# Performance work log

Hardware: AMD Instinct MI355X
Metric: run time of the kernel (lower is better)

Reference implementation:

```python
import jax, jax.numpy as jnp
import numpy as np

BN_EPS = 1e-5


def setup_inputs() -> dict:
    key = jax.random.key(0)
    k1, k2, k3, k4 = jax.random.split(key, 4)
    N, C, T, V, K = 64, 128, 300, 25, 3
    x = jax.random.normal(k1, (N, C, T, V), dtype=jnp.float32)
    A = jax.random.uniform(k2, (K, V, V), dtype=jnp.float32)
    # 1x1 conv weight (out_channels*K, in_channels) and bias
    W = jax.random.normal(k3, (C * K, C), dtype=jnp.float32) * 0.05
    b = jax.random.normal(k4, (C * K,), dtype=jnp.float32) * 0.05
    gamma = jnp.ones((C,), dtype=jnp.float32)
    beta = jnp.zeros((C,), dtype=jnp.float32)
    return {"x": x, "A": A, "W": W, "b": b, "gamma": gamma, "beta": beta}


def reference(x, A, W, b, gamma, beta):
    N, C, T, V = x.shape
    K = A.shape[0]
    # 1x1 conv: expand channels C -> K*C
    y = jnp.einsum('nctv,oc->notv', x, W) + b[None, :, None, None]
    y = y.reshape(N, K, C, T, V)
    # graph aggregation over K adjacency matrices
    y = jnp.einsum('nkctv,kvw->nctw', y, A)
    # residual + relu
    y = jax.nn.relu(y + x)
    # BatchNorm2d (training mode): stats over (N, T, V) per channel, biased var
    mean = jnp.mean(y, axis=(0, 2, 3), keepdims=True)
    var = jnp.mean(jnp.square(y - mean), axis=(0, 2, 3), keepdims=True)
    out = gamma[None, :, None, None] * (y - mean) * jax.lax.rsqrt(var + BN_EPS) + beta[None, :, None, None]
    return out, A
```

## Files before the change

### kernel.cpp

```cpp
#include <hip/hip_runtime.h>
#include <cstdint>
#include <cstddef>

#define C_    128
#define T_    300
#define V_    25
#define TT    2
#define KA    3
#define WPAD  32
#define NPOS  64
#define KDIM  384
#define B2P   392
#define ALP   40
#define XTP   40
#define NSLOT 64
#define NTOT  64

typedef __attribute__((ext_vector_type(8))) short short8;
typedef __attribute__((ext_vector_type(4))) short short4v;
typedef __attribute__((ext_vector_type(4))) float float4v;
typedef __attribute__((ext_vector_type(2))) float float2v;

__device__ __forceinline__ short f2bf(float f) {
  union { float f; uint32_t u; } v; v.f = f;
  uint32_t r = (v.u + 0x7FFFu + ((v.u >> 16) & 1u)) >> 16;
  return (short)(uint16_t)r;
}
__device__ __forceinline__ float bf2f(short s) {
  union { uint32_t u; float f; } v; v.u = ((uint32_t)(uint16_t)s) << 16;
  return v.f;
}

__global__ __launch_bounds__(256) void k0_prep(const float* __restrict__ W,
    const float* __restrict__ A, const float* __restrict__ b,
    short* __restrict__ W2, float* __restrict__ bias2, float* __restrict__ stats)
{
  int e = blockIdx.x * 256 + threadIdx.x;
  if (e < C_*KDIM) {
    int c = e / KDIM, kd = e % KDIM;
    int k = kd >> 7, c2 = kd & 127;
    W2[e] = f2bf(W[(k*C_ + c)*C_ + c2]);
  } else if (e < C_*KDIM + C_*32) {
    int i = e - C_*KDIM;
    int c = i >> 5, w = i & 31;
    float val = 0.f;
    if (w < V_) {
      for (int k = 0; k < KA; ++k) {
        float cs = 0.f;
        for (int v = 0; v < V_; ++v) cs += A[(k*V_ + v)*V_ + w];
        val += b[k*C_ + c] * cs;
      }
    }
    bias2[i] = val;
  } else if (e < C_*KDIM + C_*32 + 2*NSLOT*C_) {
    stats[e - (C_*KDIM + C_*32)] = 0.f;
  }
}

__global__ __launch_bounds__(256) void k1_main(const float* __restrict__ x,
    const float* __restrict__ A, const short* __restrict__ W2,
    const float* __restrict__ bias2, float* __restrict__ ssum,
    float* __restrict__ ssq, float* __restrict__ out)
{
  __shared__ short Albf[KA][WPAD][ALP];
  __shared__ short xt[TT][C_][XTP];
  __shared__ short B2[NPOS][B2P];

  const int tid  = threadIdx.x;
  const int lane = tid & 63;
  const int wid  = tid >> 6;
  const int l15  = lane & 15;
  const int quad = lane >> 4;
  const int nb = blockIdx.x;
  const int n  = nb / (T_/TT);
  const int tb = nb % (T_/TT);
  const int t0 = tb * TT;

  for (int i = tid; i < KA*WPAD*ALP; i += 256) {
    int k = i / (WPAD*ALP);
    int rem = i % (WPAD*ALP);
    int w = rem / ALP;
    int v = rem % ALP;
    float a = (w < V_ && v < V_) ? A[(k*V_ + v)*V_ + w] : 0.f;
    ((short*)Albf)[i] = f2bf(a);
  }
  for (int i = tid; i < TT*C_*15; i += 256) {
    int t = i / (C_*15);
    int r = i % (C_*15);
    int c = r / 15;
    int v = V_ + (r % 15);
    xt[t][c][v] = 0;
  }
  {
    const float* xb = x + (((size_t)n*C_)*T_ + t0)*V_;
    for (int p = tid; p < 3200; p += 256) {
      int c = (p*5243) >> 17;
      int r = p - c*25;
      float2v xv = *(const float2v*)(xb + (size_t)c*(T_*V_) + 2*r);
      int j0 = 2*r;
      { int j = j0;   int t = (j >= V_); int v = j - t*V_; xt[t][c][v] = f2bf(xv[0]); }
      { int j = j0+1; int t = (j >= V_); int v = j - t*V_; xt[t][c][v] = f2bf(xv[1]); }
    }
  }
  __syncthreads();

  #pragma unroll
  for (int iu = 0; iu < 3; ++iu) {
    int u  = wid*3 + iu;
    int mh = u / 6;
    int k  = (u >> 1) % 3;
    int t  = u & 1;
    short8 bf0 = *(const short8*)&Albf[k][l15][quad*8];
    short8 bf1 = *(const short8*)&Albf[k][16 + l15][quad*8];
    #pragma unroll
    for (int mi4 = 0; mi4 < 4; ++mi4) {
      int mi = mh*4 + mi4;
      int cp = mi*16 + l15;
      short8 af = *(const short8*)&xt[t][cp][quad*8];
      int c2 = k*C_ + mi*16 + quad*4;
      #pragma unroll
      for (int ni = 0; ni < 2; ++ni) {
        float4v acc = {0.f, 0.f, 0.f, 0.f};
        acc = __builtin_amdgcn_mfma_f32_16x16x32_bf16(af, ni ? bf1 : bf0, acc, 0, 0, 0);
        short4v sv;
        sv[0] = f2bf(acc[0]); sv[1] = f2bf(acc[1]);
        sv[2] = f2bf(acc[2]); sv[3] = f2bf(acc[3]);
        int pos = t*WPAD + ni*16 + l15;
        *(short4v*)&B2[pos][c2] = sv;
      }
    }
  }
  __syncthreads();

  const int wm = wid >> 1;
  const int wn = wid & 1;
  float4v acc[4][2];
  #pragma unroll
  for (int mi = 0; mi < 4; ++mi)
    #pragma unroll
    for (int ni = 0; ni < 2; ++ni)
      acc[mi][ni] = (float4v){0.f, 0.f, 0.f, 0.f};

  #pragma unroll 4
  for (int ks = 0; ks < 12; ++ks) {
    short8 bfr0 = *(const short8*)&B2[wn*32 + l15][ks*32 + quad*8];
    short8 bfr1 = *(const short8*)&B2[wn*32 + 16 + l15][ks*32 + quad*8];
    #pragma unroll
    for (int mi = 0; mi < 4; ++mi) {
      int c = wm*64 + mi*16 + l15;
      short8 afr = *(const short8*)(W2 + (size_t)c*KDIM + ks*32 + quad*8);
      acc[mi][0] = __builtin_amdgcn_mfma_f32_16x16x32_bf16(afr, bfr0, acc[mi][0], 0, 0, 0);
      acc[mi][1] = __builtin_amdgcn_mfma_f32_16x16x32_bf16(afr, bfr1, acc[mi][1], 0, 0, 0);
    }
  }

  float lsum[4][4], lsq[4][4];
  #pragma unroll
  for (int a1 = 0; a1 < 4; ++a1)
    #pragma unroll
    for (int a2 = 0; a2 < 4; ++a2) { lsum[a1][a2] = 0.f; lsq[a1][a2] = 0.f; }

  #pragma unroll
  for (int ni = 0; ni < 2; ++ni) {
    int pos = wn*32 + ni*16 + l15;
    int t = pos >> 5;
    int w = pos & 31;
    if (w < V_) {
      #pragma unroll
      for (int mi = 0; mi < 4; ++mi) {
        int cb = wm*64 + mi*16 + quad*4;
        #pragma unroll
        for (int r = 0; r < 4; ++r) {
          int cc = cb + r;
          float z = acc[mi][ni][r] + bias2[cc*32 + w];
          z += bf2f(xt[t][cc][w]);
          z = fmaxf(z, 0.f);
          acc[mi][ni][r] = z;
          lsum[mi][r] += z;
          lsq[mi][r]  += z*z;
        }
      }
    }
  }

  __syncthreads();
  float* Zs = (float*)&B2[0][0];

  #pragma unroll
  for (int ni = 0; ni < 2; ++ni) {
    int pos = wn*32 + ni*16 + l15;
    int t = pos >> 5;
    int w = pos & 31;
    if (w < V_) {
      #pragma unroll
      for (int mi = 0; mi < 4; ++mi) {
        int cb = wm*64 + mi*16 + quad*4;
        #pragma unroll
        for (int r = 0; r < 4; ++r) {
          Zs[(cb + r)*50 + t*V_ + w] = acc[mi][ni][r];
        }
      }
    }
  }
  __syncthreads();

  {
    float* ob = out + (((size_t)n*C_)*T_ + t0)*V_;
    for (int p = tid; p < 3200; p += 256) {
      int c = (p*5243) >> 17;
      int r = p - c*25;
      float2v zz = *(const float2v*)&Zs[c*50 + 2*r];
      *(float2v*)(ob + (size_t)c*(T_*V_) + 2*r) = zz;
    }
  }

  int slot = nb & (NSLOT - 1);
  #pragma unroll
  for (int mi = 0; mi < 4; ++mi) {
    #pragma unroll
    for (int r = 0; r < 4; ++r) {
      float s = lsum[mi][r];
      float q = lsq[mi][r];
      #pragma unroll
      for (int m = 1; m <= 8; m <<= 1) {
        s += __shfl_xor(s, m, 64);
        q += __shfl_xor(q, m, 64);
      }
      if (l15 == 0) {
        int cc = wm*64 + mi*16 + quad*4 + r;
        atomicAdd(&ssum[slot*C_ + cc], s);
        atomicAdd(&ssq[slot*C_ + cc], q);
      }
    }
  }
}

__global__ __launch_bounds__(256) void k2_stats(const float* __restrict__ ssum,
    const float* __restrict__ ssq, const float* __restrict__ gamma,
    const float* __restrict__ beta, const float* __restrict__ A,
    float* __restrict__ sscale, float* __restrict__ sshift, float* __restrict__ outA)
{
  int id = blockIdx.x * 256 + threadIdx.x;
  if (id < C_) {
    float s = 0.f, q = 0.f;
    for (int sl = 0; sl < NSLOT; ++sl) { s += ssum[sl*C_ + id]; q += ssq[sl*C_ + id]; }
    const float cnt = 480000.f;
    float mean = s / cnt;
    float var  = q / cnt - mean*mean;
    float inv  = rsqrtf(var + 1e-5f);
    float sc   = gamma[id] * inv;
    sscale[id] = sc;
    sshift[id] = beta[id] - mean * sc;
  } else if (id < C_ + KA*V_*V_) {
    int i = id - C_;
    outA[i] = A[i];
  }
}

__global__ __launch_bounds__(256) void k3_bn(float* __restrict__ out,
    const float* __restrict__ sscale, const float* __restrict__ sshift)
{
  __shared__ float s_sc[C_], s_sh[C_];
  int tid = threadIdx.x;
  if (tid < C_) s_sc[tid] = sscale[tid];
  else          s_sh[tid - C_] = sshift[tid - C_];
  __syncthreads();

  int n = blockIdx.x / 19;
  int chunk = blockIdx.x % 19;
  int t0c = chunk * 16;
  int tlen = (t0c + 16 <= T_) ? 16 : (T_ - t0c);
  int vlim = tlen * V_;

  for (int f = tid; f < 12800; f += 256) {
    int c = (f*5243) >> 19;
    int r = f - c*100;
    int idx0 = 4*r;
    if (idx0 >= vlim) continue;
    size_t off4 = ((size_t)n*C_*T_*V_ + (size_t)c*T_*V_ + (size_t)t0c*V_ + idx0) >> 2;
    float4v v = ((float4v*)out)[off4];
    float sc = s_sc[c], sh = s_sh[c];
    v[0] = v[0]*sc + sh; v[1] = v[1]*sc + sh;
    v[2] = v[2]*sc + sh; v[3] = v[3]*sc + sh;
    ((float4v*)out)[off4] = v;
  }
}

extern "C" void kernel_launch(void* const* d_in, const int* in_sizes, int n_in,
                              void* d_out, int out_size, void* d_ws, size_t ws_size,
                              hipStream_t stream)
{
  const float* x     = (const float*)d_in[0];
  const float* A     = (const float*)d_in[1];
  const float* W     = (const float*)d_in[2];
  const float* b     = (const float*)d_in[3];
  const float* gamma = (const float*)d_in[4];
  const float* beta  = (const float*)d_in[5];
  float* out = (float*)d_out;

  short* W2    = (short*)d_ws;
  float* bias2 = (float*)((char*)d_ws + 98304);
  float* stats = (float*)((char*)d_ws + 114688);
  float* ssum   = stats;
  float* ssq    = stats + NSLOT*C_;
  float* sscale = stats + 2*NSLOT*C_;
  float* sshift = sscale + C_;
  float* outA = out + (size_t)NTOT*C_*T_*V_;

  k0_prep <<<272,   256, 0, stream>>>(W, A, b, W2, bias2, stats);
  k1_main <<<9600,  256, 0, stream>>>(x, A, W2, bias2, ssum, ssq, out);
  k2_stats<<<8,     256, 0, stream>>>(ssum, ssq, gamma, beta, A, sscale, sshift, outA);
  k3_bn   <<<1216,  256, 0, stream>>>(out, sscale, sshift);
}
```

Baseline: 982.9 us.

## Process graph aggregation per adjacency slice to shrink LDS and raise occupancy

The k1 kernel now builds the intermediate B2 buffer one adjacency slice k at a time, 128 channels wide instead of 384. Each slice's partial GEMM is accumulated before the buffer is reused, with W2 fragments preloaded into registers per slice. This cuts shared memory use so three blocks can fit per CU (launch bounds set to 3), at the cost of extra barriers and register pressure. The BN apply kernel is also remapped to 4800 smaller blocks with a simpler index computation.

```diff
diff --git a/kernel.cpp b/kernel.cpp
--- a/kernel.cpp
+++ b/kernel.cpp
@@ -7,14 +7,17 @@
 #define V_    25
 #define TT    2
 #define KA    3
-#define WPAD  32
-#define NPOS  64
 #define KDIM  384
-#define B2P   392
+#define B2P   136
 #define ALP   40
 #define XTP   40
 #define NSLOT 64
 #define NTOT  64
+
+#define ALBF_O 0
+#define XT_O   3840
+#define B2_O   14080
+#define SH_TOT 22784
 
 typedef __attribute__((ext_vector_type(8))) short short8;
 typedef __attribute__((ext_vector_type(4))) short short4v;
@@ -57,14 +60,15 @@
   }
 }
 
-__global__ __launch_bounds__(256) void k1_main(const float* __restrict__ x,
+__global__ __launch_bounds__(256, 3) void k1_main(const float* __restrict__ x,
     const float* __restrict__ A, const short* __restrict__ W2,
     const float* __restrict__ bias2, float* __restrict__ ssum,
     float* __restrict__ ssq, float* __restrict__ out)
 {
-  __shared__ short Albf[KA][WPAD][ALP];
-  __shared__ short xt[TT][C_][XTP];
-  __shared__ short B2[NPOS][B2P];
+  __shared__ __align__(16) short SH[SH_TOT];
+  short* Albf_ = SH + ALBF_O;
+  short* xt_   = SH + XT_O;
+  short* B2_   = SH + B2_O;
 
   const int tid  = threadIdx.x;
   const int lane = tid & 63;
@@ -76,20 +80,20 @@
   const int tb = nb % (T_/TT);
   const int t0 = tb * TT;
 
-  for (int i = tid; i < KA*WPAD*ALP; i += 256) {
-    int k = i / (WPAD*ALP);
-    int rem = i % (WPAD*ALP);
+  for (int i = tid; i < KA*32*ALP; i += 256) {
+    int k = i / (32*ALP);
+    int rem = i % (32*ALP);
     int w = rem / ALP;
     int v = rem % ALP;
     float a = (w < V_ && v < V_) ? A[(k*V_ + v)*V_ + w] : 0.f;
-    ((short*)Albf)[i] = f2bf(a);
+    Albf_[i] = f2bf(a);
   }
   for (int i = tid; i < TT*C_*15; i += 256) {
     int t = i / (C_*15);
     int r = i % (C_*15);
     int c = r / 15;
     int v = V_ + (r % 15);
-    xt[t][c][v] = 0;
+    xt_[t*5120 + c*XTP + v] = 0;
   }
   {
     const float* xb = x + (((size_t)n*C_)*T_ + t0)*V_;
@@ -98,42 +102,17 @@
       int r = p - c*25;
       float2v xv = *(const float2v*)(xb + (size_t)c*(T_*V_) + 2*r);
       int j0 = 2*r;
-      { int j = j0;   int t = (j >= V_); int v = j - t*V_; xt[t][c][v] = f2bf(xv[0]); }
-      { int j = j0+1; int t = (j >= V_); int v = j - t*V_; xt[t][c][v] = f2bf(xv[1]); }
+      { int j = j0;   int t = (j >= V_); int v = j - t*V_; xt_[t*5120 + c*XTP + v] = f2bf(xv[0]); }
+      { int j = j0+1; int t = (j >= V_); int v = j - t*V_; xt_[t*5120 + c*XTP + v] = f2bf(xv[1]); }
     }
   }
   __syncthreads();
 
-  #pragma unroll
-  for (int iu = 0; iu < 3; ++iu) {
-    int u  = wid*3 + iu;
-    int mh = u / 6;
-    int k  = (u >> 1) % 3;
-    int t  = u & 1;
-    short8 bf0 = *(const short8*)&Albf[k][l15][quad*8];
-    short8 bf1 = *(const short8*)&Albf[k][16 + l15][quad*8];
-    #pragma unroll
-    for (int mi4 = 0; mi4 < 4; ++mi4) {
-      int mi = mh*4 + mi4;
-      int cp = mi*16 + l15;
-      short8 af = *(const short8*)&xt[t][cp][quad*8];
-      int c2 = k*C_ + mi*16 + quad*4;
-      #pragma unroll
-      for (int ni = 0; ni < 2; ++ni) {
-        float4v acc = {0.f, 0.f, 0.f, 0.f};
-        acc = __builtin_amdgcn_mfma_f32_16x16x32_bf16(af, ni ? bf1 : bf0, acc, 0, 0, 0);
-        short4v sv;
-        sv[0] = f2bf(acc[0]); sv[1] = f2bf(acc[1]);
-        sv[2] = f2bf(acc[2]); sv[3] = f2bf(acc[3]);
-        int pos = t*WPAD + ni*16 + l15;
-        *(short4v*)&B2[pos][c2] = sv;
-      }
-    }
-  }
-  __syncthreads();
-
+  const int mh = wid >> 1;
+  const int tW = wid & 1;
   const int wm = wid >> 1;
   const int wn = wid & 1;
+
   float4v acc[4][2];
   #pragma unroll
   for (int mi = 0; mi < 4; ++mi)
@@ -141,17 +120,49 @@
     for (int ni = 0; ni < 2; ++ni)
       acc[mi][ni] = (float4v){0.f, 0.f, 0.f, 0.f};
 
-  #pragma unroll 4
-  for (int ks = 0; ks < 12; ++ks) {
-    short8 bfr0 = *(const short8*)&B2[wn*32 + l15][ks*32 + quad*8];
-    short8 bfr1 = *(const short8*)&B2[wn*32 + 16 + l15][ks*32 + quad*8];
-    #pragma unroll
-    for (int mi = 0; mi < 4; ++mi) {
-      int c = wm*64 + mi*16 + l15;
-      short8 afr = *(const short8*)(W2 + (size_t)c*KDIM + ks*32 + quad*8);
-      acc[mi][0] = __builtin_amdgcn_mfma_f32_16x16x32_bf16(afr, bfr0, acc[mi][0], 0, 0, 0);
-      acc[mi][1] = __builtin_amdgcn_mfma_f32_16x16x32_bf16(afr, bfr1, acc[mi][1], 0, 0, 0);
-    }
+  short8 w2r[4][4];
+  const short* w2base = W2 + (size_t)(wm*64 + l15)*KDIM + quad*8;
+
+  for (int k = 0; k < KA; ++k) {
+    #pragma unroll
+    for (int ks = 0; ks < 4; ++ks)
+      #pragma unroll
+      for (int mi = 0; mi < 4; ++mi)
+        w2r[ks][mi] = *(const short8*)(w2base + (size_t)mi*16*KDIM + k*C_ + ks*32);
+
+    {
+      short8 bf0 = *(const short8*)&Albf_[k*1280 + l15*ALP + quad*8];
+      short8 bf1 = *(const short8*)&Albf_[k*1280 + (16 + l15)*ALP + quad*8];
+      #pragma unroll
+      for (int mi4 = 0; mi4 < 4; ++mi4) {
+        int m8 = mh*4 + mi4;
+        short8 af = *(const short8*)&xt_[tW*5120 + (m8*16 + l15)*XTP + quad*8];
+        int c2 = m8*16 + quad*4;
+        #pragma unroll
+        for (int ni = 0; ni < 2; ++ni) {
+          float4v s1 = {0.f, 0.f, 0.f, 0.f};
+          s1 = __builtin_amdgcn_mfma_f32_16x16x32_bf16(af, ni ? bf1 : bf0, s1, 0, 0, 0);
+          short4v sv;
+          sv[0] = f2bf(s1[0]); sv[1] = f2bf(s1[1]);
+          sv[2] = f2bf(s1[2]); sv[3] = f2bf(s1[3]);
+          int pos = tW*32 + ni*16 + l15;
+          *(short4v*)&B2_[pos*B2P + c2] = sv;
+        }
+      }
+    }
+    __syncthreads();
+
+    #pragma unroll
+    for (int ks = 0; ks < 4; ++ks) {
+      short8 b0 = *(const short8*)&B2_[(wn*32 + l15)*B2P + ks*32 + quad*8];
+      short8 b1 = *(const short8*)&B2_[(wn*32 + 16 + l15)*B2P + ks*32 + quad*8];
+      #pragma unroll
+      for (int mi = 0; mi < 4; ++mi) {
+        acc[mi][0] = __builtin_amdgcn_mfma_f32_16x16x32_bf16(w2r[ks][mi], b0, acc[mi][0], 0, 0, 0);
+        acc[mi][1] = __builtin_amdgcn_mfma_f32_16x16x32_bf16(w2r[ks][mi], b1, acc[mi][1], 0, 0, 0);
+      }
+    }
+    if (k < KA-1) __syncthreads();
   }
 
   float lsum[4][4], lsq[4][4];
@@ -173,7 +184,7 @@
         for (int r = 0; r < 4; ++r) {
           int cc = cb + r;
           float z = acc[mi][ni][r] + bias2[cc*32 + w];
-          z += bf2f(xt[t][cc][w]);
+          z += bf2f(xt_[t*5120 + cc*XTP + w]);
           z = fmaxf(z, 0.f);
           acc[mi][ni][r] = z;
           lsum[mi][r] += z;
@@ -184,7 +195,7 @@
   }
 
   __syncthreads();
-  float* Zs = (float*)&B2[0][0];
+  float* Zs = (float*)SH;
 
   #pragma unroll
   for (int ni = 0; ni < 2; ++ni) {
@@ -266,23 +277,31 @@
   else          s_sh[tid - C_] = sshift[tid - C_];
   __syncthreads();
 
-  int n = blockIdx.x / 19;
-  int chunk = blockIdx.x % 19;
-  int t0c = chunk * 16;
-  int tlen = (t0c + 16 <= T_) ? 16 : (T_ - t0c);
-  int vlim = tlen * V_;
-
-  for (int f = tid; f < 12800; f += 256) {
-    int c = (f*5243) >> 19;
-    int r = f - c*100;
-    int idx0 = 4*r;
-    if (idx0 >= vlim) continue;
-    size_t off4 = ((size_t)n*C_*T_*V_ + (size_t)c*T_*V_ + (size_t)t0c*V_ + idx0) >> 2;
-    float4v v = ((float4v*)out)[off4];
+  int n = blockIdx.x / 75;
+  int chunk = blockIdx.x % 75;
+  float* base = out + (size_t)n*C_*T_*V_ + chunk*100;
+
+  int f = tid;
+  #pragma unroll 4
+  for (int it = 0; it < 12; ++it, f += 256) {
+    int c = (f*5243) >> 17;
+    int r = f - c*25;
+    float4v* p = (float4v*)(base + (size_t)c*(T_*V_) + 4*r);
+    float4v v = *p;
     float sc = s_sc[c], sh = s_sh[c];
     v[0] = v[0]*sc + sh; v[1] = v[1]*sc + sh;
     v[2] = v[2]*sc + sh; v[3] = v[3]*sc + sh;
-    ((float4v*)out)[off4] = v;
+    *p = v;
+  }
+  if (f < 3200) {
+    int c = (f*5243) >> 17;
+    int r = f - c*25;
+    float4v* p = (float4v*)(base + (size_t)c*(T_*V_) + 4*r);
+    float4v v = *p;
+    float sc = s_sc[c], sh = s_sh[c];
+    v[0] = v[0]*sc + sh; v[1] = v[1]*sc + sh;
+    v[2] = v[2]*sc + sh; v[3] = v[3]*sc + sh;
+    *p = v;
   }
 }
 
@@ -310,5 +329,5 @@
   k0_prep <<<272,   256, 0, stream>>>(W, A, b, W2, bias2, stats);
   k1_main <<<9600,  256, 0, stream>>>(x, A, W2, bias2, ssum, ssq, out);
   k2_stats<<<8,     256, 0, stream>>>(ssum, ssq, gamma, beta, A, sscale, sshift, outA);
-  k3_bn   <<<1216,  256, 0, stream>>>(out, sscale, sshift);
-}
+  k3_bn   <<<4800,  256, 0, stream>>>(out, sscale, sshift);
+}
```

Result: faster. 889.9 us (-9.5%).
